# Performance work log

Measured on AMD Instinct MI355X. Metric: run time of the kernel, lower is better.

## Reference

```python
import jax, jax.numpy as jnp
import numpy as np

C = 64  # num_channels
B, H, W = 16, 160, 160


def squeeze2d(x, f=2):
    b, c, h, w = x.shape
    x = x.reshape(b, c, h // f, f, w // f, f)
    x = x.transpose(0, 1, 3, 5, 2, 4)
    return x.reshape(b, c * f * f, h // f, w // f)


def unsqueeze2d(x, f=2):
    b, c, h, w = x.shape
    x = x.reshape(b, c // (f * f), f, f, h, w)
    x = x.transpose(0, 1, 4, 2, 5, 3)
    return x.reshape(b, c // (f * f), h * f, w * f)


def get_indices(num_channels):
    # generate_ind(p) tiles the row-major-flattened 2x2 pattern over C//4 channel groups
    def gen(p):
        return np.tile(np.array(p, dtype=bool), num_channels // 4)
    m = np.ones(num_channels, dtype=bool)
    t = gen([0, 0, 1, 1]); b = ~t
    l = gen([0, 1, 0, 1]); r = ~l
    return (m, t, b, l, r, t & l, t & r, b & l, b & r)


INDS = get_indices(C)


def conv1x1(z, w):
    # 1x1 conv == channel matmul
    return jnp.einsum('oc,bchw->bohw', w, z)


def partition_input(x):
    z = unsqueeze2d(x)
    z = jnp.pad(z, ((0, 0), (0, 0), (1, 1), (1, 1)), constant_values=-1.0)
    z = squeeze2d(z)  # (B, C, H+1, W+1)
    m, t, b, l, r, tl, tr, bl, br = INDS
    return (z[:, :, 1:-1, 1:-1],
            z[:, t, :1, 1:-1], z[:, b, -1:, 1:-1],
            z[:, l, 1:-1, :1], z[:, r, 1:-1, -1:],
            z[:, tl, :1, :1], z[:, tr, :1, -1:],
            z[:, bl, -1:, :1], z[:, br, -1:, -1:])


def unsqueeze_line(ze):
    b, c = ze.shape[:2]
    sz = (1, -1) if ze.shape[-2] == 1 else (-1, 1)
    return ze.reshape(b, c // 2, 2, -1).transpose(0, 1, 3, 2).reshape(b, c // 2, *sz)


def merge_output(z_m, z_t, z_b, z_l, z_r, z_tl, z_tr, z_bl, z_br):
    z_m = unsqueeze2d(z_m)
    z_t, z_b, z_l, z_r = [unsqueeze_line(zi) for zi in (z_t, z_b, z_l, z_r)]
    z_tt = jnp.concatenate([z_tl, z_t, z_tr], axis=3)
    z_mm = jnp.concatenate([z_l, z_m, z_r], axis=3)
    z_bb = jnp.concatenate([z_bl, z_b, z_br], axis=3)
    return squeeze2d(jnp.concatenate([z_tt, z_mm, z_bb], axis=2))


def setup_inputs() -> dict:
    key = jax.random.key(0)
    k1, k2 = jax.random.split(key)
    x = jax.random.normal(k1, (B, C, H, W), dtype=jnp.float32)
    logdet = jax.random.normal(k2, (B,), dtype=jnp.float32)
    rng = np.random.RandomState(0)
    w_init = np.linalg.qr(rng.randn(C, C))[0].astype(np.float32)
    weight = jnp.asarray(w_init)
    return {"input": x, "logdet": logdet, "weight": weight}


def reference(input, logdet, weight):
    h, w = input.shape[-2:]
    pixels = [(h - 1) * (w - 1), w - 1, w - 1, h - 1, h - 1, 1, 1, 1, 1]
    ws = [weight[np.ix_(ind, ind)] for ind in INDS]
    dlogdet = sum(jnp.linalg.slogdet(wi)[1] * p for wi, p in zip(ws, pixels))
    zs = partition_input(input)
    outs = [conv1x1(z, wi) for z, wi in zip(zs, ws)]
    output = merge_output(*outs)
    return output, logdet + dlogdet
```

## Files before the change

### kernel.cpp

```cpp
#include <hip/hip_runtime.h>
#include <math.h>

#define NB 16
#define NC 64
#define HW 160
#define PLANE (HW * HW)
#define SG 161
#define NSITES (NB * SG * SG)
#define OUT_LD_OFF (NB * NC * PLANE)

#define SMEM_FLOATS (4096 + 1024 + 1024 + 256 + 4)

__device__ inline int chmap(int i, int n, int pa, int pb) {
    if (n == 64) return i;
    if (n == 32) return ((i >> 1) << 2) | ((i & 1) ? pb : pa);
    return (i << 2) | pa;
}

__device__ float wave_lu_logabsdet(const float* __restrict__ W, float* A,
                                   int n, int sh, int pa, int pb, int lane) {
    for (int e = lane; e < n * n; e += 64) {
        int i = e >> sh, j = e & (n - 1);
        A[e] = W[chmap(i, n, pa, pb) * 64 + chmap(j, n, pa, pb)];
    }
    asm volatile("s_waitcnt lgkmcnt(0) vmcnt(0)" ::: "memory");
    float logdet = 0.f;
    for (int k = 0; k < n; ++k) {
        float cand = -1.f;
        int idx = k;
        if (lane >= k && lane < n) {
            cand = fabsf(A[(lane << sh) + k]);
            idx = lane;
        }
        for (int off = 32; off; off >>= 1) {
            float oc = __shfl_down(cand, off, 64);
            int oi = __shfl_down(idx, off, 64);
            if (oc > cand) { cand = oc; idx = oi; }
        }
        int p = __shfl(idx, 0, 64);
        if (p != k && lane < n) {
            float tk = A[(k << sh) + lane];
            float tp = A[(p << sh) + lane];
            A[(k << sh) + lane] = tp;
            A[(p << sh) + lane] = tk;
        }
        asm volatile("s_waitcnt lgkmcnt(0)" ::: "memory");
        float piv = A[(k << sh) + k];
        logdet += logf(fabsf(piv));
        float rpiv = 1.f / piv;
        float ckj = (lane < n) ? A[(k << sh) + lane] : 0.f;
        bool act = (lane > k) && (lane < n);
        for (int i2 = k + 1; i2 < n; ++i2) {
            float aik = A[(i2 << sh) + k];
            float mult = aik * rpiv;
            if (act) A[(i2 << sh) + lane] = fmaf(-mult, ckj, A[(i2 << sh) + lane]);
        }
        asm volatile("s_waitcnt lgkmcnt(0)" ::: "memory");
    }
    return logdet;
}

__global__ __launch_bounds__(256, 4) void InvConv1x1GridAlign_kernel(
    const float* __restrict__ x, const float* __restrict__ ld_in,
    const float* __restrict__ W, float* __restrict__ out) {
    __shared__ __align__(16) float smem[SMEM_FLOATS];

    if (blockIdx.x == 0) {
        float* A64 = smem;
        float* A32a = smem + 4096;
        float* A32b = smem + 5120;
        float* A16 = smem + 6144;
        float* partial = smem + 6400;
        int wid = threadIdx.x >> 6;
        int lane = threadIdx.x & 63;
        float part = 0.f;
        if (wid == 0) {
            part = 25281.f * wave_lu_logabsdet(W, A64, 64, 6, 0, 0, lane);
        } else if (wid == 1) {
            part  = wave_lu_logabsdet(W, A32a, 32, 5, 2, 3, lane);
            part += wave_lu_logabsdet(W, A32a, 32, 5, 0, 1, lane);
            part *= 159.f;
        } else if (wid == 2) {
            part  = wave_lu_logabsdet(W, A32b, 32, 5, 1, 3, lane);
            part += wave_lu_logabsdet(W, A32b, 32, 5, 0, 2, lane);
            part *= 159.f;
        } else {
            part  = wave_lu_logabsdet(W, A16, 16, 4, 3, 0, lane);
            part += wave_lu_logabsdet(W, A16, 16, 4, 2, 0, lane);
            part += wave_lu_logabsdet(W, A16, 16, 4, 1, 0, lane);
            part += wave_lu_logabsdet(W, A16, 16, 4, 0, 0, lane);
        }
        if (lane == 0) partial[wid] = part;
        __syncthreads();
        if (threadIdx.x < NB) {
            float dl = partial[0] + partial[1] + partial[2] + partial[3];
            out[OUT_LD_OFF + threadIdx.x] = ld_in[threadIdx.x] + dl;
        }
        return;
    }

    {
        float4* dst = (float4*)smem;
        const float4* src = (const float4*)W;
        for (int i = threadIdx.x; i < 1024; i += 256) dst[i] = src[i];
    }
    __syncthreads();

    int s = (blockIdx.x - 1) * 256 + threadIdx.x;
    if (s >= NSITES) return;
    unsigned us = (unsigned)s;
    unsigned b = us / (SG * SG);
    unsigned rr = us - b * (SG * SG);
    unsigned uy = rr / SG;
    int Y = (int)uy;
    int X = (int)(rr - uy * SG);

    const float* xb = x + (size_t)b * NC * PLANE;
    float* ob = out + (size_t)b * NC * PLANE;

    bool okT = (Y >= 1), okB = (Y <= HW - 1), okL = (X >= 1), okR = (X <= HW - 1);
    bool v00 = okT && okL, v01 = okT && okR, v10 = okB && okL, v11 = okB && okR;
    int off00 = (Y - 1) * HW + (X - 1);
    int off01 = (Y - 1) * HW + X;
    int off10 = Y * HW + (X - 1);
    int off11 = Y * HW + X;

    float u[64];
#pragma unroll
    for (int o = 0; o < 64; ++o) u[o] = 0.f;

#pragma unroll 1
    for (int cc = 0; cc < 4; ++cc) {
        float v[16];
#pragma unroll
        for (int g4 = 0; g4 < 4; ++g4) {
            const float* pg = xb + (size_t)(cc * 4 + g4) * 4 * PLANE;
            v[g4 * 4 + 0] = v00 ? pg[3 * PLANE + off00] : 0.f;
            v[g4 * 4 + 1] = v01 ? pg[2 * PLANE + off01] : 0.f;
            v[g4 * 4 + 2] = v10 ? pg[1 * PLANE + off10] : 0.f;
            v[g4 * 4 + 3] = v11 ? pg[0 * PLANE + off11] : 0.f;
        }
        const float* wc = smem + cc * 16;
#pragma unroll
        for (int o = 0; o < 64; ++o) {
            const float4* wr = (const float4*)(wc + o * 64);
            float4 w0 = wr[0];
            float4 w1 = wr[1];
            float4 w2 = wr[2];
            float4 w3 = wr[3];
            float a = u[o];
            a = fmaf(w0.x, v[0], a);  a = fmaf(w0.y, v[1], a);
            a = fmaf(w0.z, v[2], a);  a = fmaf(w0.w, v[3], a);
            a = fmaf(w1.x, v[4], a);  a = fmaf(w1.y, v[5], a);
            a = fmaf(w1.z, v[6], a);  a = fmaf(w1.w, v[7], a);
            a = fmaf(w2.x, v[8], a);  a = fmaf(w2.y, v[9], a);
            a = fmaf(w2.z, v[10], a); a = fmaf(w2.w, v[11], a);
            a = fmaf(w3.x, v[12], a); a = fmaf(w3.y, v[13], a);
            a = fmaf(w3.z, v[14], a); a = fmaf(w3.w, v[15], a);
            u[o] = a;
        }
    }

#pragma unroll
    for (int g = 0; g < 16; ++g) {
        float* pg = ob + (size_t)g * 4 * PLANE;
        if (v00) pg[3 * PLANE + off00] = u[g * 4 + 0];
        if (v01) pg[2 * PLANE + off01] = u[g * 4 + 1];
        if (v10) pg[1 * PLANE + off10] = u[g * 4 + 2];
        if (v11) pg[0 * PLANE + off11] = u[g * 4 + 3];
    }
}

extern "C" void kernel_launch(void* const* d_in, const int* in_sizes, int n_in,
                              void* d_out, int out_size, void* d_ws, size_t ws_size,
                              hipStream_t stream) {
    const float* x = (const float*)d_in[0];
    const float* ld = (const float*)d_in[1];
    const float* W = (const float*)d_in[2];
    float* out = (float*)d_out;
    int nconv = (NSITES + 255) / 256;
    hipLaunchKernelGGL(InvConv1x1GridAlign_kernel, dim3(nconv + 1), dim3(256), 0,
                       stream, x, ld, W, out);
}
```

Baseline: 295.9 us.

## Restructure conv into shared-memory staged input tile with 16x4 register blocking

Each block now stages a tile of 256 sites by 32 input channels in shared memory, loaded cooperatively with each thread gathering 8 consecutive sites. Each wave then computes 16 output channels for 4 sites per lane, with the weights read from global memory as wave-uniform values. This replaces the old scheme of one site per thread with 64 accumulators and weights in LDS. The aim is to cut register pressure and LDS weight traffic and raise occupancy, at the cost of extra barriers and index arithmetic in the loads and stores.

```diff
diff --git a/kernel.cpp b/kernel.cpp
--- a/kernel.cpp
+++ b/kernel.cpp
@@ -6,10 +6,13 @@
 #define HW 160
 #define PLANE (HW * HW)
 #define SG 161
-#define NSITES (NB * SG * SG)
+#define SGSQ (SG * SG)
+#define NSITES (NB * SGSQ)
 #define OUT_LD_OFF (NB * NC * PLANE)
-
-#define SMEM_FLOATS (4096 + 1024 + 1024 + 256 + 4)
+#define TILE 256
+#define NCONV ((NSITES + TILE - 1) / TILE)
+
+#define SMEM_FLOATS (32 * 256)
 
 __device__ inline int chmap(int i, int n, int pa, int pb) {
     if (n == 64) return i;
@@ -64,6 +67,7 @@
     const float* __restrict__ x, const float* __restrict__ ld_in,
     const float* __restrict__ W, float* __restrict__ out) {
     __shared__ __align__(16) float smem[SMEM_FLOATS];
+    const int tid = threadIdx.x;
 
     if (blockIdx.x == 0) {
         float* A64 = smem;
@@ -71,8 +75,8 @@
         float* A32b = smem + 5120;
         float* A16 = smem + 6144;
         float* partial = smem + 6400;
-        int wid = threadIdx.x >> 6;
-        int lane = threadIdx.x & 63;
+        int wid = tid >> 6;
+        int lane = tid & 63;
         float part = 0.f;
         if (wid == 0) {
             part = 25281.f * wave_lu_logabsdet(W, A64, 64, 6, 0, 0, lane);
@@ -92,82 +96,110 @@
         }
         if (lane == 0) partial[wid] = part;
         __syncthreads();
-        if (threadIdx.x < NB) {
+        if (tid < NB) {
             float dl = partial[0] + partial[1] + partial[2] + partial[3];
-            out[OUT_LD_OFF + threadIdx.x] = ld_in[threadIdx.x] + dl;
+            out[OUT_LD_OFF + tid] = ld_in[tid] + dl;
         }
         return;
     }
 
+    const int tile0 = ((int)blockIdx.x - 1) * TILE;
+    const int lane = tid & 63;
+    const int wid = tid >> 6;
+    const int wo = __builtin_amdgcn_readfirstlane(wid << 4);
+
+    float acc[16][4];
+#pragma unroll
+    for (int j = 0; j < 16; ++j)
+#pragma unroll
+        for (int s2 = 0; s2 < 4; ++s2) acc[j][s2] = 0.f;
+
+    for (int half = 0; half < 2; ++half) {
+        __syncthreads();
+        {
+            const int scol = (tid & 31) << 3;
+#pragma unroll
+            for (int p = 0; p < 4; ++p) {
+                const int krow = (tid >> 5) + (p << 3);
+                const int k = (half << 5) + krow;
+                const int pl = k ^ 3;
+                const int dy = (k >> 1) & 1, dx = k & 1;
+                const int s0 = tile0 + scol;
+                unsigned us = (unsigned)s0;
+                unsigned b0 = us / SGSQ;
+                unsigned rr = us - b0 * SGSQ;
+                unsigned Y0 = rr / SG;
+                unsigned X0 = rr - Y0 * SG;
+                float vals[8];
+#pragma unroll
+                for (int j = 0; j < 8; ++j) {
+                    unsigned X = X0 + j, Y = Y0, b = b0;
+                    if (X >= SG) { X -= SG; ++Y; if (Y >= SG) { Y = 0; ++b; } }
+                    float vv = 0.f;
+                    int py = (int)Y - 1 + dy;
+                    int px = (int)X - 1 + dx;
+                    if ((s0 + j) < NSITES && (unsigned)py < HW && (unsigned)px < HW)
+                        vv = x[(size_t)b * (NC * PLANE) + (size_t)pl * PLANE +
+                               (unsigned)(py * HW + px)];
+                    vals[j] = vv;
+                }
+                float* dst = &smem[krow * 256 + scol];
+                *(float4*)(dst) = make_float4(vals[0], vals[1], vals[2], vals[3]);
+                *(float4*)(dst + 4) = make_float4(vals[4], vals[5], vals[6], vals[7]);
+            }
+        }
+        __syncthreads();
+        const float* vrow = smem + (lane << 2);
+#pragma unroll 4
+        for (int kk = 0; kk < 32; ++kk) {
+            const int k = (half << 5) + kk;
+            float w[16];
+#pragma unroll
+            for (int j = 0; j < 16; ++j) w[j] = W[(wo + j) * 64 + k];
+            const float4 v4 = *(const float4*)(vrow + (kk << 8));
+#pragma unroll
+            for (int j = 0; j < 16; ++j) {
+                acc[j][0] = fmaf(w[j], v4.x, acc[j][0]);
+                acc[j][1] = fmaf(w[j], v4.y, acc[j][1]);
+                acc[j][2] = fmaf(w[j], v4.z, acc[j][2]);
+                acc[j][3] = fmaf(w[j], v4.w, acc[j][3]);
+            }
+        }
+    }
+
+    const int sbase = tile0 + (lane << 2);
+    unsigned Ys[4], Xs[4];
+    size_t obase[4];
+    bool okv[4];
     {
-        float4* dst = (float4*)smem;
-        const float4* src = (const float4*)W;
-        for (int i = threadIdx.x; i < 1024; i += 256) dst[i] = src[i];
-    }
-    __syncthreads();
-
-    int s = (blockIdx.x - 1) * 256 + threadIdx.x;
-    if (s >= NSITES) return;
-    unsigned us = (unsigned)s;
-    unsigned b = us / (SG * SG);
-    unsigned rr = us - b * (SG * SG);
-    unsigned uy = rr / SG;
-    int Y = (int)uy;
-    int X = (int)(rr - uy * SG);
-
-    const float* xb = x + (size_t)b * NC * PLANE;
-    float* ob = out + (size_t)b * NC * PLANE;
-
-    bool okT = (Y >= 1), okB = (Y <= HW - 1), okL = (X >= 1), okR = (X <= HW - 1);
-    bool v00 = okT && okL, v01 = okT && okR, v10 = okB && okL, v11 = okB && okR;
-    int off00 = (Y - 1) * HW + (X - 1);
-    int off01 = (Y - 1) * HW + X;
-    int off10 = Y * HW + (X - 1);
-    int off11 = Y * HW + X;
-
-    float u[64];
-#pragma unroll
-    for (int o = 0; o < 64; ++o) u[o] = 0.f;
-
-#pragma unroll 1
-    for (int cc = 0; cc < 4; ++cc) {
-        float v[16];
-#pragma unroll
-        for (int g4 = 0; g4 < 4; ++g4) {
-            const float* pg = xb + (size_t)(cc * 4 + g4) * 4 * PLANE;
-            v[g4 * 4 + 0] = v00 ? pg[3 * PLANE + off00] : 0.f;
-            v[g4 * 4 + 1] = v01 ? pg[2 * PLANE + off01] : 0.f;
-            v[g4 * 4 + 2] = v10 ? pg[1 * PLANE + off10] : 0.f;
-            v[g4 * 4 + 3] = v11 ? pg[0 * PLANE + off11] : 0.f;
-        }
-        const float* wc = smem + cc * 16;
-#pragma unroll
-        for (int o = 0; o < 64; ++o) {
-            const float4* wr = (const float4*)(wc + o * 64);
-            float4 w0 = wr[0];
-            float4 w1 = wr[1];
-            float4 w2 = wr[2];
-            float4 w3 = wr[3];
-            float a = u[o];
-            a = fmaf(w0.x, v[0], a);  a = fmaf(w0.y, v[1], a);
-            a = fmaf(w0.z, v[2], a);  a = fmaf(w0.w, v[3], a);
-            a = fmaf(w1.x, v[4], a);  a = fmaf(w1.y, v[5], a);
-            a = fmaf(w1.z, v[6], a);  a = fmaf(w1.w, v[7], a);
-            a = fmaf(w2.x, v[8], a);  a = fmaf(w2.y, v[9], a);
-            a = fmaf(w2.z, v[10], a); a = fmaf(w2.w, v[11], a);
-            a = fmaf(w3.x, v[12], a); a = fmaf(w3.y, v[13], a);
-            a = fmaf(w3.z, v[14], a); a = fmaf(w3.w, v[15], a);
-            u[o] = a;
-        }
-    }
-
-#pragma unroll
-    for (int g = 0; g < 16; ++g) {
-        float* pg = ob + (size_t)g * 4 * PLANE;
-        if (v00) pg[3 * PLANE + off00] = u[g * 4 + 0];
-        if (v01) pg[2 * PLANE + off01] = u[g * 4 + 1];
-        if (v10) pg[1 * PLANE + off10] = u[g * 4 + 2];
-        if (v11) pg[0 * PLANE + off11] = u[g * 4 + 3];
+        unsigned us = (unsigned)sbase;
+        unsigned b0 = us / SGSQ;
+        unsigned rr = us - b0 * SGSQ;
+        unsigned Y0 = rr / SG;
+        unsigned X0 = rr - Y0 * SG;
+#pragma unroll
+        for (int s2 = 0; s2 < 4; ++s2) {
+            unsigned X = X0 + s2, Y = Y0, b = b0;
+            if (X >= SG) { X -= SG; ++Y; if (Y >= SG) { Y = 0; ++b; } }
+            Ys[s2] = Y;
+            Xs[s2] = X;
+            obase[s2] = (size_t)b * (NC * PLANE);
+            okv[s2] = (sbase + s2) < NSITES;
+        }
+    }
+#pragma unroll
+    for (int j = 0; j < 16; ++j) {
+        const int o = wo + j;
+        const int pl = o ^ 3;
+        const int dy = (o >> 1) & 1, dx = o & 1;
+#pragma unroll
+        for (int s2 = 0; s2 < 4; ++s2) {
+            int py = (int)Ys[s2] - 1 + dy;
+            int px = (int)Xs[s2] - 1 + dx;
+            if (okv[s2] && (unsigned)py < HW && (unsigned)px < HW)
+                out[obase[s2] + (size_t)pl * PLANE + (unsigned)(py * HW + px)] =
+                    acc[j][s2];
+        }
     }
 }
 
@@ -178,7 +210,6 @@
     const float* ld = (const float*)d_in[1];
     const float* W = (const float*)d_in[2];
     float* out = (float*)d_out;
-    int nconv = (NSITES + 255) / 256;
-    hipLaunchKernelGGL(InvConv1x1GridAlign_kernel, dim3(nconv + 1), dim3(256), 0,
+    hipLaunchKernelGGL(InvConv1x1GridAlign_kernel, dim3(NCONV + 1), dim3(256), 0,
                        stream, x, ld, W, out);
 }
```

Result: faster. 263.8 us (-10.8%).
